# Kernel optimization log

Hardware: AMD Instinct MI355X
Metric: run time of the kernel (lower is better)

## Reference

```python
import jax, jax.numpy as jnp
import numpy as np

NEG_SLOPE = 0.01  # torch F.leaky_relu default


def setup_inputs() -> dict:
    key = jax.random.key(0)
    k1, k2, k3, k4, k5 = jax.random.split(key, 5)
    N, E, IN_DIM, OUT_DIM = 100000, 1600000, 128, 64
    h = jax.random.normal(k1, (N, IN_DIM), dtype=jnp.float32)
    src = jax.random.randint(k2, (E,), 0, N, dtype=jnp.int64)
    dst = jax.random.randint(k3, (E,), 0, N, dtype=jnp.int64)
    # xavier_normal-ish scaled params
    W1 = jax.random.normal(k4, (OUT_DIM, IN_DIM), dtype=jnp.float32) * (2.0 / (IN_DIM + OUT_DIM)) ** 0.5
    Wa = jax.random.normal(k5, (1, 2 * OUT_DIM), dtype=jnp.float32) * (2.0 / (2 * OUT_DIM + 1)) ** 0.5
    return {"h": h, "src": src, "dst": dst, "W1": W1, "Wa": Wa}


def reference(h, src, dst, W1, Wa):
    N = h.shape[0]
    D = W1.shape[0]
    z = h @ W1.T  # [N, D]
    z_src = z[src]  # [E, D] gather
    z_dst = z[dst]  # [E, D] gather
    a_src, a_dst = Wa[0, :D], Wa[0, D:]
    # attn_fc(concat(z_src, z_dst)) == z_src@a_src + z_dst@a_dst
    e = z_src @ a_src + z_dst @ a_dst  # [E]
    e = jnp.where(e >= 0, e, NEG_SLOPE * e)  # leaky_relu
    # segment softmax over incoming edges of each dst node
    e_max = jax.ops.segment_max(e, dst, num_segments=N)
    e_max = jnp.where(jnp.isfinite(e_max), e_max, 0.0)  # empty segments
    e_exp = jnp.exp(e - e_max[dst])
    denom = jax.ops.segment_sum(e_exp, dst, num_segments=N)
    alpha = e_exp / jnp.maximum(denom, 1e-16)[dst]  # [E]
    # weighted scatter-sum of source messages
    h_out = jax.ops.segment_sum(alpha[:, None] * z_src, dst, num_segments=N)  # [N, D]
    return h_out
```

## Files before the change

kernel.cpp:

```cpp
#include <hip/hip_runtime.h>
#include <hip/hip_bf16.h>

#define NEG_SLOPE 0.01f
#define NPB 512
#define CHUNK 4096

typedef __attribute__((ext_vector_type(8))) short short8;
typedef __attribute__((ext_vector_type(4))) float f32x4;

__device__ __forceinline__ unsigned short f2bf_rne(float f) {
    unsigned u = __float_as_uint(f);
    u += 0x7FFFu + ((u >> 16) & 1u);
    return (unsigned short)(u >> 16);
}

__global__ __launch_bounds__(256, 4) void k_gp(
    const float* __restrict__ h, const float* __restrict__ W1,
    const float* __restrict__ Wa, unsigned short* __restrict__ zb,
    float* __restrict__ s, float* __restrict__ t, int N, int G1,
    const int* __restrict__ src, const int* __restrict__ dst,
    unsigned* __restrict__ gcur, unsigned* __restrict__ table,
    int E, int NBKT, int BCAP)
{
    __shared__ __align__(16) union SM {
        short wsb[64 * 128];
        struct {
            unsigned cnt[256]; unsigned exc[256]; unsigned sbuf[256];
            unsigned gbaseb[256]; unsigned stage[CHUNK];
            unsigned short bkt[CHUNK];
        } p;
    } sm;
    const int tid = threadIdx.x;

    if (blockIdx.x < (unsigned)G1) {
        const int nb = blockIdx.x * 64;
        const int w  = tid >> 6;
        const int l  = tid & 63;
        const int lr = l & 15;
        const int lc = l >> 4;
        const int myn = nb + w * 16 + lr;
        const float4* __restrict__ h4 = (const float4*)h;
        const float4* __restrict__ W14 = (const float4*)W1;

        float4 av[4][2];
#pragma unroll
        for (int ks = 0; ks < 4; ++ks) {
            const int kcb = ks * 4 + lc;
            if (myn < N) {
                av[ks][0] = h4[(size_t)myn * 32 + kcb * 2];
                av[ks][1] = h4[(size_t)myn * 32 + kcb * 2 + 1];
            } else {
                av[ks][0] = make_float4(0.f, 0.f, 0.f, 0.f);
                av[ks][1] = make_float4(0.f, 0.f, 0.f, 0.f);
            }
        }

#pragma unroll
        for (int it = 0; it < 4; ++it) {
            const int q = tid + it * 256;
            const int r = q >> 4, cb = q & 15;
            float4 v0 = W14[(size_t)r * 32 + cb * 2];
            float4 v1 = W14[(size_t)r * 32 + cb * 2 + 1];
            short8 o;
            o[0]=f2bf_rne(v0.x); o[1]=f2bf_rne(v0.y); o[2]=f2bf_rne(v0.z); o[3]=f2bf_rne(v0.w);
            o[4]=f2bf_rne(v1.x); o[5]=f2bf_rne(v1.y); o[6]=f2bf_rne(v1.z); o[7]=f2bf_rne(v1.w);
            *(short8*)&sm.wsb[r * 128 + ((cb * 8) ^ ((r & 7) << 3))] = o;
        }
        __syncthreads();

        f32x4 acc[4];
#pragma unroll
        for (int ni = 0; ni < 4; ++ni) acc[ni] = (f32x4){0.f, 0.f, 0.f, 0.f};

#pragma unroll
        for (int ks = 0; ks < 4; ++ks) {
            const int kcb = ks * 4 + lc;
            short8 af;
            af[0]=f2bf_rne(av[ks][0].x); af[1]=f2bf_rne(av[ks][0].y);
            af[2]=f2bf_rne(av[ks][0].z); af[3]=f2bf_rne(av[ks][0].w);
            af[4]=f2bf_rne(av[ks][1].x); af[5]=f2bf_rne(av[ks][1].y);
            af[6]=f2bf_rne(av[ks][1].z); af[7]=f2bf_rne(av[ks][1].w);
#pragma unroll
            for (int ni = 0; ni < 4; ++ni) {
                const int wr = ni * 16 + lr;
                const short8 bf = *(const short8*)&sm.wsb[wr * 128 + ((kcb * 8) ^ ((wr & 7) << 3))];
                acc[ni] = __builtin_amdgcn_mfma_f32_16x16x32_bf16(af, bf, acc[ni], 0, 0, 0);
            }
        }

        {
            float asrc[4], adst[4];
#pragma unroll
            for (int ni = 0; ni < 4; ++ni) {
                asrc[ni] = Wa[ni * 16 + lr];
                adst[ni] = Wa[64 + ni * 16 + lr];
            }
#pragma unroll
            for (int r = 0; r < 4; ++r) {
                float ps = 0.f, pt = 0.f;
#pragma unroll
                for (int ni = 0; ni < 4; ++ni) {
                    ps = fmaf(acc[ni][r], asrc[ni], ps);
                    pt = fmaf(acc[ni][r], adst[ni], pt);
                }
#pragma unroll
                for (int m = 1; m < 16; m <<= 1) {
                    ps += __shfl_xor(ps, m);
                    pt += __shfl_xor(pt, m);
                }
                const int node = nb + w * 16 + lc * 4 + r;
                if (lr == 0 && node < N) { s[node] = ps; t[node] = pt; }
            }
        }

        __syncthreads();
#pragma unroll
        for (int ni = 0; ni < 4; ++ni) {
            const int col = ni * 16 + lr;
#pragma unroll
            for (int r = 0; r < 4; ++r) {
                const int row = w * 16 + lc * 4 + r;
                sm.wsb[row * 64 + (((col >> 3) ^ (row & 7)) << 3) + (col & 7)]
                    = (short)f2bf_rne(acc[ni][r]);
            }
        }
        __syncthreads();
        {
            const int r = tid >> 2;
            const int n = nb + r;
            if (n < N) {
#pragma unroll
                for (int j = 0; j < 2; ++j) {
                    const int c = (tid & 3) * 2 + j;
                    const short8 v = *(const short8*)&sm.wsb[r * 64 + ((c ^ (r & 7)) << 3)];
                    *(short8*)&zb[(size_t)n * 64 + c * 8] = v;
                }
            }
        }
    } else {
        const int e0 = (blockIdx.x - G1) * CHUNK;
        const int nE = min(CHUNK, E - e0);

        sm.p.cnt[tid] = 0u;
        __syncthreads();
        for (int i = tid; i < nE; i += 256)
            atomicAdd(&sm.p.cnt[(unsigned)dst[e0 + i] >> 9], 1u);
        __syncthreads();

        const unsigned myc = sm.p.cnt[tid];
        if (tid < NBKT && myc > 0u) sm.p.gbaseb[tid] = atomicAdd(&gcur[tid], myc);

        sm.p.sbuf[tid] = myc;
        __syncthreads();
        for (int off = 1; off < 256; off <<= 1) {
            unsigned x = (tid >= off) ? sm.p.sbuf[tid - off] : 0u;
            __syncthreads();
            sm.p.sbuf[tid] += x;
            __syncthreads();
        }
        sm.p.exc[tid] = sm.p.sbuf[tid] - myc;
        __syncthreads();
        sm.p.cnt[tid] = 0u;
        __syncthreads();

        for (int i = tid; i < nE; i += 256) {
            const unsigned d = (unsigned)dst[e0 + i];
            const unsigned b = d >> 9;
            const unsigned pos = sm.p.exc[b] + atomicAdd(&sm.p.cnt[b], 1u);
            sm.p.stage[pos] = ((unsigned)src[e0 + i] << 9) | (d & 511u);
            sm.p.bkt[pos] = (unsigned short)b;
        }
        __syncthreads();

        for (int i = tid; i < nE; i += 256) {
            const unsigned b = sm.p.bkt[i];
            const unsigned off = sm.p.gbaseb[b] + ((unsigned)i - sm.p.exc[b]);
            if (off < (unsigned)BCAP)
                table[(size_t)b * BCAP + off] = sm.p.stage[i];
        }
    }
}

__global__ __launch_bounds__(256) void k_sortb2(
    const unsigned* __restrict__ table, const unsigned* __restrict__ gcur,
    unsigned* __restrict__ edge_src,
    unsigned* __restrict__ offsets, unsigned* __restrict__ counts,
    int N, int NBKT, int BCAP)
{
    __shared__ unsigned ncnt[NPB];
    __shared__ unsigned nexc[NPB];
    __shared__ unsigned sbuf[NPB];
    __shared__ unsigned basesh;
    const int b = blockIdx.x;
    const int t = threadIdx.x;
    const int bc = min((int)gcur[b], BCAP);
    const size_t tb = (size_t)b * BCAP;

    {
        unsigned c = (t < NBKT) ? min(gcur[t], (unsigned)BCAP) : 0u;
        sbuf[t] = c;
        __syncthreads();
        for (int off = 1; off < 256; off <<= 1) {
            unsigned x = (t >= off) ? sbuf[t - off] : 0u;
            __syncthreads();
            sbuf[t] += x;
            __syncthreads();
        }
        if (t == 0) basesh = (b == 0) ? 0u : sbuf[b - 1];
        __syncthreads();
    }
    const unsigned base = basesh;
    __syncthreads();

    ncnt[t] = 0u; ncnt[t + 256] = 0u;
    __syncthreads();
    for (int i = t; i < bc; i += 256)
        atomicAdd(&ncnt[table[tb + i] & 511u], 1u);
    __syncthreads();

    const unsigned c0 = ncnt[t], c1 = ncnt[t + 256];
    sbuf[t] = c0; sbuf[t + 256] = c1;
    __syncthreads();
    for (int off = 1; off < NPB; off <<= 1) {
        unsigned x0 = (t >= off) ? sbuf[t - off] : 0u;
        unsigned x1 = (t + 256 >= off) ? sbuf[t + 256 - off] : 0u;
        __syncthreads();
        sbuf[t] += x0; sbuf[t + 256] += x1;
        __syncthreads();
    }
    nexc[t] = sbuf[t] - c0; nexc[t + 256] = sbuf[t + 256] - c1;
    __syncthreads();

    {
        const int n0 = b * NPB + t, n1 = n0 + 256;
        if (n0 < N) { offsets[n0] = base + nexc[t];        counts[n0] = c0; }
        if (n1 < N) { offsets[n1] = base + nexc[t + 256];  counts[n1] = c1; }
    }
    ncnt[t] = 0u; ncnt[t + 256] = 0u;
    __syncthreads();

    for (int i = t; i < bc; i += 256) {
        const unsigned v = table[tb + i];
        const unsigned l = v & 511u;
        const unsigned pos = nexc[l] + atomicAdd(&ncnt[l], 1u);
        edge_src[base + pos] = v >> 9;
    }
}

__global__ __launch_bounds__(256) void k_node(
    const unsigned* __restrict__ offsets, const unsigned* __restrict__ counts,
    const unsigned* __restrict__ edge_src,
    const float* __restrict__ s, const float* __restrict__ t,
    const unsigned short* __restrict__ zb, float* __restrict__ out, int N)
{
    const int tid = threadIdx.x;
    const int node = blockIdx.x * 16 + (tid >> 4);
    if (node >= N) return;
    const int wl    = tid & 63;
    const int gbase = wl & ~15;
    const int sub   = wl & 15;
    const int g2    = sub >> 3;
    const int l8    = sub & 7;

    const unsigned beg = offsets[node];
    const int cnt = (int)counts[node];
    if (cnt == 0) {
        if (sub < 8) {
            const float4 zz = make_float4(0.f, 0.f, 0.f, 0.f);
            *(float4*)&out[(size_t)node * 64 + sub * 8]     = zz;
            *(float4*)&out[(size_t)node * 64 + sub * 8 + 4] = zz;
        }
        return;
    }

    const float tn = t[node];
    const unsigned short* __restrict__ zrow = zb + l8 * 8;
    float dl = 0.f;
    float acc[8] = {0.f, 0.f, 0.f, 0.f, 0.f, 0.f, 0.f, 0.f};

    for (int base = 0; base < cnt; base += 16) {
        const int rem = min(16, cnt - base);
        int sj = 0;
        float p = 0.f;
        if (sub < rem) {
            sj = (int)edge_src[beg + base + sub];
            float e = s[sj] + tn;
            e = (e >= 0.f) ? e : NEG_SLOPE * e;
            p = __expf(e);
            dl += p;
        }
#pragma unroll
        for (int k = 0; k < 8; ++k) {
            const int j = g2 * 8 + k;
            const float pj  = __shfl(p, gbase + j);
            const int   sjj = __shfl(sj, gbase + j);
            const uint4 v = *(const uint4*)&zrow[(size_t)sjj * 64];
#define UNPK(u, d0) \
            acc[d0]     = fmaf(pj, __uint_as_float((u) << 16),          acc[d0]); \
            acc[d0 + 1] = fmaf(pj, __uint_as_float((u) & 0xFFFF0000u), acc[d0 + 1]);
            UNPK(v.x, 0) UNPK(v.y, 2) UNPK(v.z, 4) UNPK(v.w, 6)
#undef UNPK
        }
    }

#pragma unroll
    for (int c = 0; c < 8; ++c)
        acc[c] += __shfl_xor(acc[c], 8);
    float den = dl;
#pragma unroll
    for (int m = 1; m < 16; m <<= 1) den += __shfl_xor(den, m);

    if (sub < 8) {
        const float inv = 1.f / fmaxf(den, 1e-16f);
        float4 o0 = make_float4(acc[0] * inv, acc[1] * inv, acc[2] * inv, acc[3] * inv);
        float4 o1 = make_float4(acc[4] * inv, acc[5] * inv, acc[6] * inv, acc[7] * inv);
        *(float4*)&out[(size_t)node * 64 + sub * 8]     = o0;
        *(float4*)&out[(size_t)node * 64 + sub * 8 + 4] = o1;
    }
}

extern "C" void kernel_launch(void* const* d_in, const int* in_sizes, int n_in,
                              void* d_out, int out_size, void* d_ws, size_t ws_size,
                              hipStream_t stream) {
    const float* h   = (const float*)d_in[0];
    const int*   src = (const int*)d_in[1];
    const int*   dst = (const int*)d_in[2];
    const float* W1  = (const float*)d_in[3];
    const float* Wa  = (const float*)d_in[4];
    float* out = (float*)d_out;

    const int N = in_sizes[0] / 128;
    const int E = in_sizes[1];
    const int NBKT = (N + NPB - 1) / NPB;
    const int meanb = (E + NBKT - 1) / NBKT;
    int slack = 24 * (int)sqrtf((float)meanb) + 64;
    const int BCAP = meanb + slack;

    const int G1 = (N + 63) / 64;
    const int G2 = (E + CHUNK - 1) / CHUNK;

    unsigned short* zb = (unsigned short*)d_ws;
    float*    s        = (float*)(zb + (size_t)N * 64);
    float*    t        = s + N;
    unsigned* gcur     = (unsigned*)(t + N);
    unsigned* offsets  = gcur + NBKT;
    unsigned* counts   = offsets + N;
    unsigned* edge_src = counts + N;
    unsigned* table    = edge_src + E;

    hipMemsetAsync(gcur, 0, (size_t)NBKT * sizeof(unsigned), stream);

    k_gp<<<G1 + G2, 256, 0, stream>>>(h, W1, Wa, zb, s, t, N, G1,
                                      src, dst, gcur, table, E, NBKT, BCAP);
    k_sortb2<<<NBKT, 256, 0, stream>>>(table, gcur, edge_src, offsets, counts, N, NBKT, BCAP);
    k_node<<<(N + 15) / 16, 256, 0, stream>>>(offsets, counts, edge_src, s, t, zb, out, N);
}
```

Before: 103.9 us.

## Process 256 nodes per GEMM block with per-wave row loop and prefetch

Each projection block now handles 256 nodes instead of 64: each wave loops over four 16-row groups, reusing the bf16 W1 tile staged once in shared memory. The next group's h rows are loaded while the current group's MFMAs run, and output staging uses a per-wave LDS buffer, so the block-wide syncs around the store go away. This cuts the redundant W1 loads and conversions per node by four and makes the GEMM blocks a quarter as many, at the cost of more registers and LDS per block and less parallelism on the GEMM side.

```diff
diff --git a/kernel.cpp b/kernel.cpp
--- a/kernel.cpp
+++ b/kernel.cpp
@@ -23,7 +23,7 @@
     int E, int NBKT, int BCAP)
 {
     __shared__ __align__(16) union SM {
-        short wsb[64 * 128];
+        struct { short wsb[64 * 128]; short tbuf[4][16 * 64]; } g;
         struct {
             unsigned cnt[256]; unsigned exc[256]; unsigned sbuf[256];
             unsigned gbaseb[256]; unsigned stage[CHUNK];
@@ -33,25 +33,35 @@
     const int tid = threadIdx.x;
 
     if (blockIdx.x < (unsigned)G1) {
-        const int nb = blockIdx.x * 64;
+        const int nb = blockIdx.x * 256;
         const int w  = tid >> 6;
         const int l  = tid & 63;
         const int lr = l & 15;
         const int lc = l >> 4;
-        const int myn = nb + w * 16 + lr;
+        const int rowbase = nb + w * 64;
         const float4* __restrict__ h4 = (const float4*)h;
         const float4* __restrict__ W14 = (const float4*)W1;
 
-        float4 av[4][2];
-#pragma unroll
-        for (int ks = 0; ks < 4; ++ks) {
-            const int kcb = ks * 4 + lc;
-            if (myn < N) {
-                av[ks][0] = h4[(size_t)myn * 32 + kcb * 2];
-                av[ks][1] = h4[(size_t)myn * 32 + kcb * 2 + 1];
-            } else {
-                av[ks][0] = make_float4(0.f, 0.f, 0.f, 0.f);
-                av[ks][1] = make_float4(0.f, 0.f, 0.f, 0.f);
+        float asrc[4], adst[4];
+#pragma unroll
+        for (int ni = 0; ni < 4; ++ni) {
+            asrc[ni] = Wa[ni * 16 + lr];
+            adst[ni] = Wa[64 + ni * 16 + lr];
+        }
+
+        float4 av[8];
+        {
+            const int myn = rowbase + lr;
+#pragma unroll
+            for (int ks = 0; ks < 4; ++ks) {
+                const int kcb = ks * 4 + lc;
+                if (myn < N) {
+                    av[2 * ks]     = h4[(size_t)myn * 32 + kcb * 2];
+                    av[2 * ks + 1] = h4[(size_t)myn * 32 + kcb * 2 + 1];
+                } else {
+                    av[2 * ks]     = make_float4(0.f, 0.f, 0.f, 0.f);
+                    av[2 * ks + 1] = make_float4(0.f, 0.f, 0.f, 0.f);
+                }
             }
         }
 
@@ -64,37 +74,52 @@
             short8 o;
             o[0]=f2bf_rne(v0.x); o[1]=f2bf_rne(v0.y); o[2]=f2bf_rne(v0.z); o[3]=f2bf_rne(v0.w);
             o[4]=f2bf_rne(v1.x); o[5]=f2bf_rne(v1.y); o[6]=f2bf_rne(v1.z); o[7]=f2bf_rne(v1.w);
-            *(short8*)&sm.wsb[r * 128 + ((cb * 8) ^ ((r & 7) << 3))] = o;
-        }
-        __syncthreads();
-
-        f32x4 acc[4];
-#pragma unroll
-        for (int ni = 0; ni < 4; ++ni) acc[ni] = (f32x4){0.f, 0.f, 0.f, 0.f};
-
-#pragma unroll
-        for (int ks = 0; ks < 4; ++ks) {
-            const int kcb = ks * 4 + lc;
-            short8 af;
-            af[0]=f2bf_rne(av[ks][0].x); af[1]=f2bf_rne(av[ks][0].y);
-            af[2]=f2bf_rne(av[ks][0].z); af[3]=f2bf_rne(av[ks][0].w);
-            af[4]=f2bf_rne(av[ks][1].x); af[5]=f2bf_rne(av[ks][1].y);
-            af[6]=f2bf_rne(av[ks][1].z); af[7]=f2bf_rne(av[ks][1].w);
-#pragma unroll
-            for (int ni = 0; ni < 4; ++ni) {
-                const int wr = ni * 16 + lr;
-                const short8 bf = *(const short8*)&sm.wsb[wr * 128 + ((kcb * 8) ^ ((wr & 7) << 3))];
-                acc[ni] = __builtin_amdgcn_mfma_f32_16x16x32_bf16(af, bf, acc[ni], 0, 0, 0);
-            }
-        }
-
-        {
-            float asrc[4], adst[4];
-#pragma unroll
-            for (int ni = 0; ni < 4; ++ni) {
-                asrc[ni] = Wa[ni * 16 + lr];
-                adst[ni] = Wa[64 + ni * 16 + lr];
-            }
+            *(short8*)&sm.g.wsb[r * 128 + ((cb * 8) ^ ((r & 7) << 3))] = o;
+        }
+        __syncthreads();
+
+        short* __restrict__ tb = sm.g.tbuf[w];
+
+#pragma unroll
+        for (int rg = 0; rg < 4; ++rg) {
+            short8 afr[4];
+#pragma unroll
+            for (int ks = 0; ks < 4; ++ks) {
+                const float4 v0 = av[2 * ks], v1 = av[2 * ks + 1];
+                short8 o;
+                o[0]=f2bf_rne(v0.x); o[1]=f2bf_rne(v0.y); o[2]=f2bf_rne(v0.z); o[3]=f2bf_rne(v0.w);
+                o[4]=f2bf_rne(v1.x); o[5]=f2bf_rne(v1.y); o[6]=f2bf_rne(v1.z); o[7]=f2bf_rne(v1.w);
+                afr[ks] = o;
+            }
+            if (rg < 3) {
+                const int myn = rowbase + (rg + 1) * 16 + lr;
+#pragma unroll
+                for (int ks = 0; ks < 4; ++ks) {
+                    const int kcb = ks * 4 + lc;
+                    if (myn < N) {
+                        av[2 * ks]     = h4[(size_t)myn * 32 + kcb * 2];
+                        av[2 * ks + 1] = h4[(size_t)myn * 32 + kcb * 2 + 1];
+                    } else {
+                        av[2 * ks]     = make_float4(0.f, 0.f, 0.f, 0.f);
+                        av[2 * ks + 1] = make_float4(0.f, 0.f, 0.f, 0.f);
+                    }
+                }
+            }
+
+            f32x4 acc[4];
+#pragma unroll
+            for (int ni = 0; ni < 4; ++ni) acc[ni] = (f32x4){0.f, 0.f, 0.f, 0.f};
+#pragma unroll
+            for (int ks = 0; ks < 4; ++ks) {
+                const int kcb = ks * 4 + lc;
+#pragma unroll
+                for (int ni = 0; ni < 4; ++ni) {
+                    const int wr = ni * 16 + lr;
+                    const short8 bf = *(const short8*)&sm.g.wsb[wr * 128 + ((kcb * 8) ^ ((wr & 7) << 3))];
+                    acc[ni] = __builtin_amdgcn_mfma_f32_16x16x32_bf16(afr[ks], bf, acc[ni], 0, 0, 0);
+                }
+            }
+
 #pragma unroll
             for (int r = 0; r < 4; ++r) {
                 float ps = 0.f, pt = 0.f;
@@ -108,32 +133,30 @@
                     ps += __shfl_xor(ps, m);
                     pt += __shfl_xor(pt, m);
                 }
-                const int node = nb + w * 16 + lc * 4 + r;
+                const int node = rowbase + rg * 16 + lc * 4 + r;
                 if (lr == 0 && node < N) { s[node] = ps; t[node] = pt; }
             }
-        }
-
-        __syncthreads();
-#pragma unroll
-        for (int ni = 0; ni < 4; ++ni) {
-            const int col = ni * 16 + lr;
-#pragma unroll
-            for (int r = 0; r < 4; ++r) {
-                const int row = w * 16 + lc * 4 + r;
-                sm.wsb[row * 64 + (((col >> 3) ^ (row & 7)) << 3) + (col & 7)]
-                    = (short)f2bf_rne(acc[ni][r]);
-            }
-        }
-        __syncthreads();
-        {
-            const int r = tid >> 2;
-            const int n = nb + r;
-            if (n < N) {
-#pragma unroll
-                for (int j = 0; j < 2; ++j) {
-                    const int c = (tid & 3) * 2 + j;
-                    const short8 v = *(const short8*)&sm.wsb[r * 64 + ((c ^ (r & 7)) << 3)];
-                    *(short8*)&zb[(size_t)n * 64 + c * 8] = v;
+
+#pragma unroll
+            for (int ni = 0; ni < 4; ++ni) {
+                const int col = ni * 16 + lr;
+#pragma unroll
+                for (int r = 0; r < 4; ++r) {
+                    const int ro = lc * 4 + r;
+                    tb[ro * 64 + (((col >> 3) ^ (ro & 7)) << 3) + (col & 7)]
+                        = (short)f2bf_rne(acc[ni][r]);
+                }
+            }
+            {
+                const int ro = l >> 2;
+                const int n = rowbase + rg * 16 + ro;
+                if (n < N) {
+#pragma unroll
+                    for (int j = 0; j < 2; ++j) {
+                        const int c = (l & 3) * 2 + j;
+                        const short8 v = *(const short8*)&tb[ro * 64 + ((c ^ (ro & 7)) << 3)];
+                        *(short8*)&zb[(size_t)n * 64 + c * 8] = v;
+                    }
                 }
             }
         }
@@ -336,7 +359,7 @@
     int slack = 24 * (int)sqrtf((float)meanb) + 64;
     const int BCAP = meanb + slack;
 
-    const int G1 = (N + 63) / 64;
+    const int G1 = (N + 255) / 256;
     const int G2 = (E + CHUNK - 1) / CHUNK;
 
     unsigned short* zb = (unsigned short*)d_ws;
```

Measured after the change: 99.15 us. 4.6% less time.
